# Kernel tuning notes

Measured on AMD Instinct MI355X. Metric: run time of the kernel, lower is better.

The kernel has to match this reference:

```python
import jax, jax.numpy as jnp
import numpy as np

N = 50000          # nodes
E = 1000000        # candidate edges (pairs within distance threshold)
ED = 32            # embed_dim = bbox_embed // 2
H = 128            # hidden_dim
C = 26             # number_of_edge_classes


def setup_inputs() -> dict:
    key = jax.random.key(0)
    ks = jax.random.split(key, 20)
    s = 0.05
    return {
        # node / edge data
        "orientation": jax.random.randint(ks[0], (N,), 0, 24, dtype=jnp.int32),
        "dimension": jax.random.uniform(ks[1], (N, 3), dtype=jnp.float32),
        "location": jax.random.normal(ks[2], (N, 3), dtype=jnp.float32),
        "src": jax.random.randint(ks[3], (E,), 0, N, dtype=jnp.int32),
        "dst": jax.random.randint(ks[4], (E,), 0, N, dtype=jnp.int32),
        "targets": jax.random.randint(ks[5], (E,), 0, C + 1, dtype=jnp.int32),
        # parameters (Linear stored as [in, out])
        "orient_table": jax.random.normal(ks[6], (24, ED), dtype=jnp.float32) * s,
        "size_W": jax.random.normal(ks[7], (3, ED), dtype=jnp.float32) * s,
        "size_b": jnp.zeros((ED,), jnp.float32),
        "subj_W": jax.random.normal(ks[8], (2 * ED, H), dtype=jnp.float32) * s,
        "subj_b": jnp.zeros((H,), jnp.float32),
        "obj_W": jax.random.normal(ks[9], (2 * ED, H), dtype=jnp.float32) * s,
        "obj_b": jnp.zeros((H,), jnp.float32),
        "trans_W": jax.random.normal(ks[10], (3, H), dtype=jnp.float32) * s,
        "trans_b": jnp.zeros((H,), jnp.float32),
        "mlp_W1": jax.random.normal(ks[11], (3 * H, 2 * H), dtype=jnp.float32) * s,
        "mlp_b1": jnp.zeros((2 * H,), jnp.float32),
        "mlp_W2": jax.random.normal(ks[12], (2 * H, H), dtype=jnp.float32) * s,
        "mlp_b2": jnp.zeros((H,), jnp.float32),
        "mlp_W3": jax.random.normal(ks[13], (H, C + 1), dtype=jnp.float32) * s,
        "mlp_b3": jnp.zeros((C + 1,), jnp.float32),
    }


def reference(orientation, dimension, location, src, dst, targets,
              orient_table, size_W, size_b, subj_W, subj_b, obj_W, obj_b,
              trans_W, trans_b, mlp_W1, mlp_b1, mlp_W2, mlp_b2, mlp_W3, mlp_b3):
    # per-node embeddings (computed once, not per pair as in the torch loop)
    orient_e = orient_table[orientation]                     # [N, ED]
    dim_e = dimension @ size_W + size_b                      # [N, ED]
    node_cat = jnp.concatenate([dim_e, orient_e], axis=-1)   # [N, 2*ED]
    subj = node_cat @ subj_W + subj_b                        # [N, H]
    obj = node_cat @ obj_W + obj_b                           # [N, H]

    # per-edge relative translation embed
    rel = (location[src] - location[dst]) @ trans_W + trans_b  # [E, H]

    # gather + concat + MLP per candidate edge
    edge_in = jnp.concatenate([subj[src], rel, obj[dst]], axis=-1)  # [E, 3H]
    h = jax.nn.relu(edge_in @ mlp_W1 + mlp_b1)               # [E, 2H]
    h = jax.nn.relu(h @ mlp_W2 + mlp_b2)                     # [E, H]
    scores = h @ mlp_W3 + mlp_b3                             # [E, C+1]
    return scores, targets
```

## Files before the change

kernel.cpp:

```cpp
#include <hip/hip_runtime.h>
#include <hip/hip_bf16.h>

#define N_NODES 50000
#define N_EDGES 1000000
#define NCLS 27

typedef short s8v __attribute__((ext_vector_type(8)));
typedef float f4v __attribute__((ext_vector_type(4)));

__device__ __forceinline__ ushort f2bf(float f) {
    __hip_bfloat16 h = __float2bfloat16(f);
    return *reinterpret_cast<ushort*>(&h);
}

__global__ __launch_bounds__(256) void k_cat(
    const int* __restrict__ ori, const float* __restrict__ dim,
    const float* __restrict__ otab, const float* __restrict__ sW,
    const float* __restrict__ sb, ushort* __restrict__ cat)
{
    const int t = threadIdx.x;
    const int n = blockIdx.x * 4 + (t >> 6);
    const int c = t & 63;
    float v;
    if (c < 32)
        v = sb[c] + dim[n*3]*sW[c] + dim[n*3+1]*sW[32+c] + dim[n*3+2]*sW[64+c];
    else
        v = otab[ori[n]*32 + (c-32)];
    cat[n*64 + c] = f2bf(v);
}

__global__ __launch_bounds__(256) void k_fold(
    const float* __restrict__ subj_W, const float* __restrict__ obj_W,
    const float* __restrict__ W1, ushort* __restrict__ SWp, ushort* __restrict__ OWp)
{
    const int idx = blockIdx.x * 256 + threadIdx.x;
    const int which = idx >> 14;
    const int e = idx & 16383;
    const int k = e >> 8;
    const int n = e & 255;
    const float* A = which ? obj_W : subj_W;
    const float* B = which ? (W1 + 256*256) : W1;
    float s = 0.f;
    for (int q = 0; q < 128; ++q) s += A[k*128 + q] * B[q*256 + n];
    const int ks = k >> 5, j = k & 7, hi = (k >> 3) & 3, nt = n >> 4, lo = n & 15;
    ushort* P = which ? OWp : SWp;
    P[((ks*16 + nt)*64 + hi*16 + lo)*8 + j] = f2bf(s);
}

__global__ __launch_bounds__(256) void k_trans(
    const float* __restrict__ trans_W, const float* __restrict__ trans_b,
    const float* __restrict__ subj_b, const float* __restrict__ obj_b,
    const float* __restrict__ W1, const float* __restrict__ b1,
    float* __restrict__ TW1, float* __restrict__ b1p)
{
    const int n = threadIdx.x;
    float t0 = 0, t1 = 0, t2 = 0, bb = b1[n];
    for (int q = 0; q < 128; ++q) {
        const float wb = W1[(128 + q)*256 + n];
        t0 += trans_W[q]       * wb;
        t1 += trans_W[128 + q] * wb;
        t2 += trans_W[256 + q] * wb;
        bb += trans_b[q] * wb;
        bb += subj_b[q] * W1[q*256 + n];
        bb += obj_b[q]  * W1[(256 + q)*256 + n];
    }
    TW1[n] = t0; TW1[256 + n] = t1; TW1[512 + n] = t2; b1p[n] = bb;
}

__global__ __launch_bounds__(256) void k_pack23(
    const float* __restrict__ W2, const float* __restrict__ W3,
    ushort* __restrict__ W2p, ushort* __restrict__ W3p)
{
    const int idx = blockIdx.x * 256 + threadIdx.x;
    if (idx < 32768) {
        const int g = idx >> 9, k = g >> 3, nt = g & 7;
        const int lane = (idx >> 3) & 63, j = idx & 7;
        W2p[idx] = f2bf(W2[(k*32 + (lane >> 4)*8 + j)*128 + nt*16 + (lane & 15)]);
    } else {
        const int e = idx - 32768;
        const int g = e >> 9, k = g >> 1, nt = g & 1;
        const int lane = (e >> 3) & 63, j = e & 7;
        const int col = nt*16 + (lane & 15);
        const int r = k*32 + (lane >> 4)*8 + j;
        W3p[e] = f2bf((col < NCLS) ? W3[r*NCLS + col] : 0.f);
    }
}

__global__ __launch_bounds__(256) void edge_mfma(
    const float* __restrict__ loc, const int* __restrict__ src, const int* __restrict__ dst,
    const ushort* __restrict__ cat, const ushort* __restrict__ SWp, const ushort* __restrict__ OWp,
    const ushort* __restrict__ W2p, const ushort* __restrict__ W3p,
    const float* __restrict__ TW1, const float* __restrict__ b1p,
    const float* __restrict__ b2, const float* __restrict__ b3,
    float* __restrict__ out)
{
    __shared__ ushort h[16384];
    __shared__ float diffs[64][4];

    const int t = threadIdx.x, lane = t & 63, w = t >> 6;
    const int lo = lane & 15, hi = lane >> 4;
    const int eb = blockIdx.x * 64;

    if (t < 64) {
        const int s = src[eb + t], d = dst[eb + t];
        diffs[t][0] = loc[s*3]     - loc[d*3];
        diffs[t][1] = loc[s*3 + 1] - loc[d*3 + 1];
        diffs[t][2] = loc[s*3 + 2] - loc[d*3 + 2];
    }
    int sidx[4], didx[4];
#pragma unroll
    for (int m = 0; m < 4; ++m) {
        sidx[m] = src[eb + m*16 + lo];
        didx[m] = dst[eb + m*16 + lo];
    }
    __syncthreads();

    const s8v* catv = (const s8v*)cat;
    const s8v* swv  = (const s8v*)SWp;
    const s8v* owv  = (const s8v*)OWp;

    f4v acc1[4][4];
#pragma unroll
    for (int m = 0; m < 4; ++m)
#pragma unroll
        for (int nt = 0; nt < 4; ++nt) acc1[m][nt] = (f4v){0.f, 0.f, 0.f, 0.f};

    s8v As[4][2], Ao[4][2];
#pragma unroll
    for (int m = 0; m < 4; ++m) {
        As[m][0] = catv[sidx[m]*8 + hi];     As[m][1] = catv[sidx[m]*8 + 4 + hi];
        Ao[m][0] = catv[didx[m]*8 + hi];     Ao[m][1] = catv[didx[m]*8 + 4 + hi];
    }
    s8v Bs[2][4], Bo[2][4];
#pragma unroll
    for (int ks = 0; ks < 2; ++ks)
#pragma unroll
        for (int nt = 0; nt < 4; ++nt) {
            Bs[ks][nt] = swv[(ks*16 + w*4 + nt)*64 + lane];
            Bo[ks][nt] = owv[(ks*16 + w*4 + nt)*64 + lane];
        }
#pragma unroll
    for (int m = 0; m < 4; ++m)
#pragma unroll
        for (int nt = 0; nt < 4; ++nt) {
            acc1[m][nt] = __builtin_amdgcn_mfma_f32_16x16x32_bf16(As[m][0], Bs[0][nt], acc1[m][nt], 0, 0, 0);
            acc1[m][nt] = __builtin_amdgcn_mfma_f32_16x16x32_bf16(As[m][1], Bs[1][nt], acc1[m][nt], 0, 0, 0);
            acc1[m][nt] = __builtin_amdgcn_mfma_f32_16x16x32_bf16(Ao[m][0], Bo[0][nt], acc1[m][nt], 0, 0, 0);
            acc1[m][nt] = __builtin_amdgcn_mfma_f32_16x16x32_bf16(Ao[m][1], Bo[1][nt], acc1[m][nt], 0, 0, 0);
        }

    float tw0[4], tw1[4], tw2[4], bia[4];
#pragma unroll
    for (int nt = 0; nt < 4; ++nt) {
        const int col = w*64 + nt*16 + lo;
        tw0[nt] = TW1[col]; tw1[nt] = TW1[256 + col]; tw2[nt] = TW1[512 + col];
        bia[nt] = b1p[col];
    }
#pragma unroll
    for (int m = 0; m < 4; ++m)
#pragma unroll
        for (int r = 0; r < 4; ++r) {
            const int row = m*16 + hi*4 + r;
            const float d0 = diffs[row][0], d1 = diffs[row][1], d2 = diffs[row][2];
#pragma unroll
            for (int nt = 0; nt < 4; ++nt) {
                float v = acc1[m][nt][r] + bia[nt] + d0*tw0[nt] + d1*tw1[nt] + d2*tw2[nt];
                v = fmaxf(v, 0.f);
                const int col = w*64 + nt*16 + lo;
                const int addr = (row*512 + col*2) ^ ((row & 7) << 4);
                *(ushort*)((char*)h + addr) = f2bf(v);
            }
        }
    __syncthreads();

    f4v acc2[4][2];
#pragma unroll
    for (int m = 0; m < 4; ++m)
#pragma unroll
        for (int nt = 0; nt < 2; ++nt) acc2[m][nt] = (f4v){0.f, 0.f, 0.f, 0.f};

    const s8v* w2v = (const s8v*)W2p;
#pragma unroll
    for (int k = 0; k < 8; ++k) {
        s8v a[4], b[2];
#pragma unroll
        for (int m = 0; m < 4; ++m) {
            const int row = m*16 + lo;
            const int addr = (row*512 + k*64 + hi*16) ^ ((row & 7) << 4);
            a[m] = *(const s8v*)((char*)h + addr);
        }
#pragma unroll
        for (int nt = 0; nt < 2; ++nt) b[nt] = w2v[(k*8 + w*2 + nt)*64 + lane];
#pragma unroll
        for (int m = 0; m < 4; ++m)
#pragma unroll
            for (int nt = 0; nt < 2; ++nt)
                acc2[m][nt] = __builtin_amdgcn_mfma_f32_16x16x32_bf16(a[m], b[nt], acc2[m][nt], 0, 0, 0);
    }
    __syncthreads();

    {
        float b2v[2];
#pragma unroll
        for (int nt = 0; nt < 2; ++nt) b2v[nt] = b2[w*32 + nt*16 + lo];
#pragma unroll
        for (int m = 0; m < 4; ++m)
#pragma unroll
            for (int nt = 0; nt < 2; ++nt)
#pragma unroll
                for (int r = 0; r < 4; ++r) {
                    const int row = m*16 + hi*4 + r;
                    const int col = w*32 + nt*16 + lo;
                    const float v = fmaxf(acc2[m][nt][r] + b2v[nt], 0.f);
                    const int addr = (row*256 + col*2) ^ ((row & 7) << 4);
                    *(ushort*)((char*)h + addr) = f2bf(v);
                }
    }
    __syncthreads();

    f4v acc3[2];
#pragma unroll
    for (int nt = 0; nt < 2; ++nt) acc3[nt] = (f4v){0.f, 0.f, 0.f, 0.f};
    const s8v* w3v = (const s8v*)W3p;
#pragma unroll
    for (int k = 0; k < 4; ++k) {
        const int row = w*16 + lo;
        const int addr = (row*256 + k*64 + hi*16) ^ ((row & 7) << 4);
        const s8v a = *(const s8v*)((char*)h + addr);
#pragma unroll
        for (int nt = 0; nt < 2; ++nt) {
            const s8v b = w3v[(k*2 + nt)*64 + lane];
            acc3[nt] = __builtin_amdgcn_mfma_f32_16x16x32_bf16(a, b, acc3[nt], 0, 0, 0);
        }
    }
#pragma unroll
    for (int nt = 0; nt < 2; ++nt) {
        const int col = nt*16 + lo;
        if (col < NCLS) {
            const float bb = b3[col];
#pragma unroll
            for (int r = 0; r < 4; ++r) {
                const int e = eb + w*16 + hi*4 + r;
                out[(size_t)e*NCLS + col] = acc3[nt][r] + bb;
            }
        }
    }
}

__global__ __launch_bounds__(256) void targets_copy_kernel(
    const int* __restrict__ targets, float* __restrict__ out_tail, int n)
{
    const int i = blockIdx.x * blockDim.x + threadIdx.x;
    if (i < n) out_tail[i] = (float)targets[i];
}

extern "C" void kernel_launch(void* const* d_in, const int* in_sizes, int n_in,
                              void* d_out, int out_size, void* d_ws, size_t ws_size,
                              hipStream_t stream) {
    const int*   orientation  = (const int*)  d_in[0];
    const float* dimension    = (const float*)d_in[1];
    const float* location     = (const float*)d_in[2];
    const int*   src          = (const int*)  d_in[3];
    const int*   dst          = (const int*)  d_in[4];
    const int*   targets      = (const int*)  d_in[5];
    const float* orient_table = (const float*)d_in[6];
    const float* size_W       = (const float*)d_in[7];
    const float* size_b       = (const float*)d_in[8];
    const float* subj_W       = (const float*)d_in[9];
    const float* obj_W        = (const float*)d_in[11];
    const float* trans_W      = (const float*)d_in[13];
    const float* trans_b      = (const float*)d_in[14];
    const float* W1           = (const float*)d_in[15];
    const float* b1           = (const float*)d_in[16];
    const float* W2           = (const float*)d_in[17];
    const float* b2           = (const float*)d_in[18];
    const float* W3           = (const float*)d_in[19];
    const float* b3           = (const float*)d_in[20];
    const float* subj_b       = (const float*)d_in[10];
    const float* obj_b        = (const float*)d_in[12];

    char* ws = (char*)d_ws;
    ushort* cat = (ushort*)(ws);
    ushort* SWp = (ushort*)(ws + 6400000);
    ushort* OWp = (ushort*)(ws + 6432768);
    ushort* W2p = (ushort*)(ws + 6465536);
    ushort* W3p = (ushort*)(ws + 6531072);
    float*  TW1 = (float*) (ws + 6539264);
    float*  b1p = (float*) (ws + 6542336);
    float*  out = (float*)d_out;

    k_cat   <<<12500, 256, 0, stream>>>(orientation, dimension, orient_table,
                                        size_W, size_b, cat);
    k_fold  <<<128,   256, 0, stream>>>(subj_W, obj_W, W1, SWp, OWp);
    k_trans <<<1,     256, 0, stream>>>(trans_W, trans_b, subj_b, obj_b, W1, b1,
                                        TW1, b1p);
    k_pack23<<<144,   256, 0, stream>>>(W2, W3, W2p, W3p);

    edge_mfma<<<N_EDGES / 64, 256, 0, stream>>>(
        location, src, dst, cat, SWp, OWp, W2p, W3p, TW1, b1p, b2, b3, out);

    targets_copy_kernel<<<(N_EDGES + 255) / 256, 256, 0, stream>>>(
        targets, out + (size_t)N_EDGES * NCLS, N_EDGES);
}
```

Measured before the change: 522.9 us.

## Fuse prep kernels, fold translation/bias into MFMA, preload weights, vectorize targets copy

Result: slower. 1.003 ms (+91.7%).

```diff
diff --git a/kernel.cpp b/kernel.cpp
--- a/kernel.cpp
+++ b/kernel.cpp
@@ -13,80 +13,76 @@
     return *reinterpret_cast<ushort*>(&h);
 }
 
-__global__ __launch_bounds__(256) void k_cat(
+__global__ __launch_bounds__(256) void k_prep(
     const int* __restrict__ ori, const float* __restrict__ dim,
     const float* __restrict__ otab, const float* __restrict__ sW,
-    const float* __restrict__ sb, ushort* __restrict__ cat)
-{
-    const int t = threadIdx.x;
-    const int n = blockIdx.x * 4 + (t >> 6);
-    const int c = t & 63;
-    float v;
-    if (c < 32)
-        v = sb[c] + dim[n*3]*sW[c] + dim[n*3+1]*sW[32+c] + dim[n*3+2]*sW[64+c];
-    else
-        v = otab[ori[n]*32 + (c-32)];
-    cat[n*64 + c] = f2bf(v);
-}
-
-__global__ __launch_bounds__(256) void k_fold(
-    const float* __restrict__ subj_W, const float* __restrict__ obj_W,
-    const float* __restrict__ W1, ushort* __restrict__ SWp, ushort* __restrict__ OWp)
-{
-    const int idx = blockIdx.x * 256 + threadIdx.x;
-    const int which = idx >> 14;
-    const int e = idx & 16383;
-    const int k = e >> 8;
-    const int n = e & 255;
-    const float* A = which ? obj_W : subj_W;
-    const float* B = which ? (W1 + 256*256) : W1;
-    float s = 0.f;
-    for (int q = 0; q < 128; ++q) s += A[k*128 + q] * B[q*256 + n];
-    const int ks = k >> 5, j = k & 7, hi = (k >> 3) & 3, nt = n >> 4, lo = n & 15;
-    ushort* P = which ? OWp : SWp;
-    P[((ks*16 + nt)*64 + hi*16 + lo)*8 + j] = f2bf(s);
-}
-
-__global__ __launch_bounds__(256) void k_trans(
+    const float* __restrict__ sb,
+    const float* __restrict__ subj_W, const float* __restrict__ subj_b,
+    const float* __restrict__ obj_W,  const float* __restrict__ obj_b,
     const float* __restrict__ trans_W, const float* __restrict__ trans_b,
-    const float* __restrict__ subj_b, const float* __restrict__ obj_b,
     const float* __restrict__ W1, const float* __restrict__ b1,
-    float* __restrict__ TW1, float* __restrict__ b1p)
-{
-    const int n = threadIdx.x;
-    float t0 = 0, t1 = 0, t2 = 0, bb = b1[n];
-    for (int q = 0; q < 128; ++q) {
-        const float wb = W1[(128 + q)*256 + n];
-        t0 += trans_W[q]       * wb;
-        t1 += trans_W[128 + q] * wb;
-        t2 += trans_W[256 + q] * wb;
-        bb += trans_b[q] * wb;
-        bb += subj_b[q] * W1[q*256 + n];
-        bb += obj_b[q]  * W1[(256 + q)*256 + n];
-    }
-    TW1[n] = t0; TW1[256 + n] = t1; TW1[512 + n] = t2; b1p[n] = bb;
-}
-
-__global__ __launch_bounds__(256) void k_pack23(
     const float* __restrict__ W2, const float* __restrict__ W3,
+    ushort* __restrict__ cat, ushort* __restrict__ SWp, ushort* __restrict__ OWp,
+    float* __restrict__ TW1, float* __restrict__ b1p,
     ushort* __restrict__ W2p, ushort* __restrict__ W3p)
 {
-    const int idx = blockIdx.x * 256 + threadIdx.x;
-    if (idx < 32768) {
-        const int g = idx >> 9, k = g >> 3, nt = g & 7;
-        const int lane = (idx >> 3) & 63, j = idx & 7;
-        W2p[idx] = f2bf(W2[(k*32 + (lane >> 4)*8 + j)*128 + nt*16 + (lane & 15)]);
+    const int b = blockIdx.x, t = threadIdx.x;
+    if (b < 3125) {
+#pragma unroll
+        for (int it = 0; it < 4; ++it) {
+            const int n = b * 16 + it * 4 + (t >> 6);
+            const int c = t & 63;
+            float v;
+            if (c < 32)
+                v = sb[c] + dim[n*3]*sW[c] + dim[n*3+1]*sW[32+c] + dim[n*3+2]*sW[64+c];
+            else
+                v = otab[ori[n]*32 + (c - 32)];
+            cat[n*64 + c] = f2bf(v);
+        }
+    } else if (b < 3253) {
+        const int idx = (b - 3125) * 256 + t;
+        const int which = idx >> 14;
+        const int e = idx & 16383;
+        const int k = e >> 8;
+        const int n = e & 255;
+        const float* A = which ? obj_W : subj_W;
+        const float* B = which ? (W1 + 256*256) : W1;
+        float s = 0.f;
+        for (int q = 0; q < 128; ++q) s += A[k*128 + q] * B[q*256 + n];
+        const int ks = k >> 5, j = k & 7, hi = (k >> 3) & 3, nt = n >> 4, lo = n & 15;
+        ushort* P = which ? OWp : SWp;
+        P[((ks*16 + nt)*64 + hi*16 + lo)*8 + j] = f2bf(s);
+    } else if (b == 3253) {
+        const int n = t;
+        float t0 = 0, t1 = 0, t2 = 0, bb = b1[n];
+        for (int q = 0; q < 128; ++q) {
+            const float wb = W1[(128 + q)*256 + n];
+            t0 += trans_W[q]       * wb;
+            t1 += trans_W[128 + q] * wb;
+            t2 += trans_W[256 + q] * wb;
+            bb += trans_b[q] * wb;
+            bb += subj_b[q] * W1[q*256 + n];
+            bb += obj_b[q]  * W1[(256 + q)*256 + n];
+        }
+        TW1[n] = t0; TW1[256 + n] = t1; TW1[512 + n] = t2; b1p[n] = bb;
     } else {
-        const int e = idx - 32768;
-        const int g = e >> 9, k = g >> 1, nt = g & 1;
-        const int lane = (e >> 3) & 63, j = e & 7;
-        const int col = nt*16 + (lane & 15);
-        const int r = k*32 + (lane >> 4)*8 + j;
-        W3p[e] = f2bf((col < NCLS) ? W3[r*NCLS + col] : 0.f);
-    }
-}
-
-__global__ __launch_bounds__(256) void edge_mfma(
+        const int idx = (b - 3254) * 256 + t;
+        if (idx < 32768) {
+            const int g = idx >> 9, k = g >> 3, nt = g & 7;
+            const int lane = (idx >> 3) & 63, j = idx & 7;
+            W2p[idx] = f2bf(W2[(k*32 + (lane >> 4)*8 + j)*128 + nt*16 + (lane & 15)]);
+        } else {
+            const int e = idx - 32768;
+            const int g = e >> 9, k = g >> 1, nt = g & 1;
+            const int lane = (e >> 3) & 63, j = e & 7;
+            const int col = nt*16 + (lane & 15);
+            const int r = k*32 + (lane >> 4)*8 + j;
+            W3p[e] = f2bf((col < NCLS) ? W3[r*NCLS + col] : 0.f);
+        }
+    }
+}
+
+__global__ __launch_bounds__(256, 4) void edge_mfma(
     const float* __restrict__ loc, const int* __restrict__ src, const int* __restrict__ dst,
     const ushort* __restrict__ cat, const ushort* __restrict__ SWp, const ushort* __restrict__ OWp,
     const ushort* __restrict__ W2p, const ushort* __restrict__ W3p,
@@ -113,24 +109,13 @@
         sidx[m] = src[eb + m*16 + lo];
         didx[m] = dst[eb + m*16 + lo];
     }
-    __syncthreads();
 
     const s8v* catv = (const s8v*)cat;
     const s8v* swv  = (const s8v*)SWp;
     const s8v* owv  = (const s8v*)OWp;
-
-    f4v acc1[4][4];
-#pragma unroll
-    for (int m = 0; m < 4; ++m)
-#pragma unroll
-        for (int nt = 0; nt < 4; ++nt) acc1[m][nt] = (f4v){0.f, 0.f, 0.f, 0.f};
-
-    s8v As[4][2], Ao[4][2];
-#pragma unroll
-    for (int m = 0; m < 4; ++m) {
-        As[m][0] = catv[sidx[m]*8 + hi];     As[m][1] = catv[sidx[m]*8 + 4 + hi];
-        Ao[m][0] = catv[didx[m]*8 + hi];     Ao[m][1] = catv[didx[m]*8 + 4 + hi];
-    }
+    const s8v* w2v  = (const s8v*)W2p;
+    const s8v* w3v  = (const s8v*)W3p;
+
     s8v Bs[2][4], Bo[2][4];
 #pragma unroll
     for (int ks = 0; ks < 2; ++ks)
@@ -139,33 +124,92 @@
             Bs[ks][nt] = swv[(ks*16 + w*4 + nt)*64 + lane];
             Bo[ks][nt] = owv[(ks*16 + w*4 + nt)*64 + lane];
         }
+    s8v w2f[8][2];
+#pragma unroll
+    for (int k = 0; k < 8; ++k)
+#pragma unroll
+        for (int nt = 0; nt < 2; ++nt)
+            w2f[k][nt] = w2v[(k*8 + w*2 + nt)*64 + lane];
+    s8v w3f[4][2];
+#pragma unroll
+    for (int k = 0; k < 4; ++k)
+#pragma unroll
+        for (int nt = 0; nt < 2; ++nt)
+            w3f[k][nt] = w3v[(k*2 + nt)*64 + lane];
+
+    s8v Bx[4];
+#pragma unroll
+    for (int nt = 0; nt < 4; ++nt) {
+        s8v bx = (s8v){0,0,0,0,0,0,0,0};
+        if (hi == 0) {
+            const int col = w*64 + nt*16 + lo;
+            bx[0] = (short)f2bf(TW1[col]);
+            bx[1] = (short)f2bf(TW1[256 + col]);
+            bx[2] = (short)f2bf(TW1[512 + col]);
+            bx[3] = (short)f2bf(b1p[col]);
+        }
+        Bx[nt] = bx;
+    }
+
+    s8v As[4][2], Ao[4][2];
+#pragma unroll
+    for (int m = 0; m < 4; ++m) {
+        As[m][0] = catv[(size_t)sidx[m]*8 + hi];
+        As[m][1] = catv[(size_t)sidx[m]*8 + 4 + hi];
+        Ao[m][0] = catv[(size_t)didx[m]*8 + hi];
+        Ao[m][1] = catv[(size_t)didx[m]*8 + 4 + hi];
+    }
+
+    f4v acc1[4][4];
 #pragma unroll
     for (int m = 0; m < 4; ++m)
 #pragma unroll
-        for (int nt = 0; nt < 4; ++nt) {
-            acc1[m][nt] = __builtin_amdgcn_mfma_f32_16x16x32_bf16(As[m][0], Bs[0][nt], acc1[m][nt], 0, 0, 0);
-            acc1[m][nt] = __builtin_amdgcn_mfma_f32_16x16x32_bf16(As[m][1], Bs[1][nt], acc1[m][nt], 0, 0, 0);
-            acc1[m][nt] = __builtin_amdgcn_mfma_f32_16x16x32_bf16(Ao[m][0], Bo[0][nt], acc1[m][nt], 0, 0, 0);
-            acc1[m][nt] = __builtin_amdgcn_mfma_f32_16x16x32_bf16(Ao[m][1], Bo[1][nt], acc1[m][nt], 0, 0, 0);
-        }
-
-    float tw0[4], tw1[4], tw2[4], bia[4];
-#pragma unroll
-    for (int nt = 0; nt < 4; ++nt) {
-        const int col = w*64 + nt*16 + lo;
-        tw0[nt] = TW1[col]; tw1[nt] = TW1[256 + col]; tw2[nt] = TW1[512 + col];
-        bia[nt] = b1p[col];
-    }
+        for (int nt = 0; nt < 4; ++nt) acc1[m][nt] = (f4v){0.f, 0.f, 0.f, 0.f};
+
+#pragma unroll
+    for (int ks = 0; ks < 2; ++ks)
+#pragma unroll
+        for (int m = 0; m < 4; ++m)
+#pragma unroll
+            for (int nt = 0; nt < 4; ++nt)
+                acc1[m][nt] = __builtin_amdgcn_mfma_f32_16x16x32_bf16(As[m][ks], Bs[ks][nt], acc1[m][nt], 0, 0, 0);
+#pragma unroll
+    for (int ks = 0; ks < 2; ++ks)
+#pragma unroll
+        for (int m = 0; m < 4; ++m)
+#pragma unroll
+            for (int nt = 0; nt < 4; ++nt)
+                acc1[m][nt] = __builtin_amdgcn_mfma_f32_16x16x32_bf16(Ao[m][ks], Bo[ks][nt], acc1[m][nt], 0, 0, 0);
+
+    __syncthreads();
+
+    s8v Ax[4];
+#pragma unroll
+    for (int m = 0; m < 4; ++m) {
+        s8v ax = (s8v){0,0,0,0,0,0,0,0};
+        if (hi == 0) {
+            const int row = m*16 + lo;
+            ax[0] = (short)f2bf(diffs[row][0]);
+            ax[1] = (short)f2bf(diffs[row][1]);
+            ax[2] = (short)f2bf(diffs[row][2]);
+            ax[3] = (short)0x3F80;
+        }
+        Ax[m] = ax;
+    }
+#pragma unroll
+    for (int m = 0; m < 4; ++m)
+#pragma unroll
+        for (int nt = 0; nt < 4; ++nt)
+            acc1[m][nt] = __builtin_amdgcn_mfma_f32_16x16x32_bf16(Ax[m], Bx[nt], acc1[m][nt], 0, 0, 0);
+
 #pragma unroll
     for (int m = 0; m < 4; ++m)
 #pragma unroll
         for (int r = 0; r < 4; ++r) {
             const int row = m*16 + hi*4 + r;
-            const float d0 = diffs[row][0], d1 = diffs[row][1], d2 = diffs[row][2];
 #pragma unroll
             for (int nt = 0; nt < 4; ++nt) {
-                float v = acc1[m][nt][r] + bia[nt] + d0*tw0[nt] + d1*tw1[nt] + d2*tw2[nt];
-                v = fmaxf(v, 0.f);
+                const float v = fmaxf(acc1[m][nt][r], 0.f);
                 const int col = w*64 + nt*16 + lo;
                 const int addr = (row*512 + col*2) ^ ((row & 7) << 4);
                 *(ushort*)((char*)h + addr) = f2bf(v);
@@ -178,11 +222,9 @@
     for (int m = 0; m < 4; ++m)
 #pragma unroll
         for (int nt = 0; nt < 2; ++nt) acc2[m][nt] = (f4v){0.f, 0.f, 0.f, 0.f};
-
-    const s8v* w2v = (const s8v*)W2p;
 #pragma unroll
     for (int k = 0; k < 8; ++k) {
-        s8v a[4], b[2];
+        s8v a[4];
 #pragma unroll
         for (int m = 0; m < 4; ++m) {
             const int row = m*16 + lo;
@@ -190,12 +232,10 @@
             a[m] = *(const s8v*)((char*)h + addr);
         }
 #pragma unroll
-        for (int nt = 0; nt < 2; ++nt) b[nt] = w2v[(k*8 + w*2 + nt)*64 + lane];
-#pragma unroll
         for (int m = 0; m < 4; ++m)
 #pragma unroll
             for (int nt = 0; nt < 2; ++nt)
-                acc2[m][nt] = __builtin_amdgcn_mfma_f32_16x16x32_bf16(a[m], b[nt], acc2[m][nt], 0, 0, 0);
+                acc2[m][nt] = __builtin_amdgcn_mfma_f32_16x16x32_bf16(a[m], w2f[k][nt], acc2[m][nt], 0, 0, 0);
     }
     __syncthreads();
 
@@ -221,17 +261,14 @@
     f4v acc3[2];
 #pragma unroll
     for (int nt = 0; nt < 2; ++nt) acc3[nt] = (f4v){0.f, 0.f, 0.f, 0.f};
-    const s8v* w3v = (const s8v*)W3p;
 #pragma unroll
     for (int k = 0; k < 4; ++k) {
         const int row = w*16 + lo;
         const int addr = (row*256 + k*64 + hi*16) ^ ((row & 7) << 4);
         const s8v a = *(const s8v*)((char*)h + addr);
 #pragma unroll
-        for (int nt = 0; nt < 2; ++nt) {
-            const s8v b = w3v[(k*2 + nt)*64 + lane];
-            acc3[nt] = __builtin_amdgcn_mfma_f32_16x16x32_bf16(a, b, acc3[nt], 0, 0, 0);
-        }
+        for (int nt = 0; nt < 2; ++nt)
+            acc3[nt] = __builtin_amdgcn_mfma_f32_16x16x32_bf16(a, w3f[k][nt], acc3[nt], 0, 0, 0);
     }
 #pragma unroll
     for (int nt = 0; nt < 2; ++nt) {
@@ -247,11 +284,16 @@
     }
 }
 
-__global__ __launch_bounds__(256) void targets_copy_kernel(
-    const int* __restrict__ targets, float* __restrict__ out_tail, int n)
+__global__ __launch_bounds__(256) void targets_copy4(
+    const int* __restrict__ targets, float* __restrict__ out_tail)
 {
     const int i = blockIdx.x * blockDim.x + threadIdx.x;
-    if (i < n) out_tail[i] = (float)targets[i];
+    if (i < N_EDGES / 4) {
+        const int4 v = ((const int4*)targets)[i];
+        float4 r;
+        r.x = (float)v.x; r.y = (float)v.y; r.z = (float)v.z; r.w = (float)v.w;
+        ((float4*)out_tail)[i] = r;
+    }
 }
 
 extern "C" void kernel_launch(void* const* d_in, const int* in_sizes, int n_in,
@@ -267,7 +309,9 @@
     const float* size_W       = (const float*)d_in[7];
     const float* size_b       = (const float*)d_in[8];
     const float* subj_W       = (const float*)d_in[9];
+    const float* subj_b       = (const float*)d_in[10];
     const float* obj_W        = (const float*)d_in[11];
+    const float* obj_b        = (const float*)d_in[12];
     const float* trans_W      = (const float*)d_in[13];
     const float* trans_b      = (const float*)d_in[14];
     const float* W1           = (const float*)d_in[15];
@@ -276,8 +320,6 @@
     const float* b2           = (const float*)d_in[18];
     const float* W3           = (const float*)d_in[19];
     const float* b3           = (const float*)d_in[20];
-    const float* subj_b       = (const float*)d_in[10];
-    const float* obj_b        = (const float*)d_in[12];
 
     char* ws = (char*)d_ws;
     ushort* cat = (ushort*)(ws);
@@ -289,16 +331,15 @@
     float*  b1p = (float*) (ws + 6542336);
     float*  out = (float*)d_out;
 
-    k_cat   <<<12500, 256, 0, stream>>>(orientation, dimension, orient_table,
-                                        size_W, size_b, cat);
-    k_fold  <<<128,   256, 0, stream>>>(subj_W, obj_W, W1, SWp, OWp);
-    k_trans <<<1,     256, 0, stream>>>(trans_W, trans_b, subj_b, obj_b, W1, b1,
-                                        TW1, b1p);
-    k_pack23<<<144,   256, 0, stream>>>(W2, W3, W2p, W3p);
+    k_prep<<<3398, 256, 0, stream>>>(
+        orientation, dimension, orient_table, size_W, size_b,
+        subj_W, subj_b, obj_W, obj_b, trans_W, trans_b,
+        W1, b1, W2, W3,
+        cat, SWp, OWp, TW1, b1p, W2p, W3p);
 
     edge_mfma<<<N_EDGES / 64, 256, 0, stream>>>(
         location, src, dst, cat, SWp, OWp, W2p, W3p, TW1, b1p, b2, b3, out);
 
-    targets_copy_kernel<<<(N_EDGES + 255) / 256, 256, 0, stream>>>(
-        targets, out + (size_t)N_EDGES * NCLS, N_EDGES);
-}
+    targets_copy4<<<(N_EDGES / 4 + 255) / 256, 256, 0, stream>>>(
+        targets, out + (size_t)N_EDGES * NCLS);
+}
```
